# Optimization experiments

Measured on AMD Instinct MI355X. Metric: run time of the kernel, lower is better.

Reference implementation:

```python
import jax, jax.numpy as jnp
import numpy as np

N_NODES = 100000


def setup_inputs() -> dict:
    key = jax.random.key(0)
    k1, k2, k3, k4 = jax.random.split(key, 4)
    E = 1600000
    in_dim, out_dim = 256, 64
    h = jax.random.normal(k1, (N_NODES, in_dim), dtype=jnp.float32)
    src = jax.random.randint(k2, (E,), 0, N_NODES, dtype=jnp.int64)
    dst = jax.random.randint(k3, (E,), 0, N_NODES, dtype=jnp.int64)
    W = jax.random.normal(k4, (in_dim, out_dim), dtype=jnp.float32) * (1.0 / np.sqrt(in_dim))
    b = jnp.zeros((out_dim,), dtype=jnp.float32)
    return {"h": h, "src": src, "dst": dst, "W": W, "b": b}


def reference(h, src, dst, W, b):
    # dgl GraphConv, norm='both': out = D_in^{-1/2} A D_out^{-1/2} h W + b
    E = src.shape[0]
    ones = jnp.ones((E,), dtype=h.dtype)
    deg_out = jax.ops.segment_sum(ones, src, num_segments=N_NODES)  # out-degree of src nodes
    deg_in = jax.ops.segment_sum(ones, dst, num_segments=N_NODES)   # in-degree of dst nodes
    norm_src = jnp.clip(deg_out, 1.0, None) ** -0.5                  # [N]
    norm_dst = jnp.clip(deg_in, 1.0, None) ** -0.5                   # [N]
    # in_dim > out_dim: project first (as dgl does), then aggregate small features
    x = (h * norm_src[:, None]) @ W                                  # [N, out_dim]
    msgs = x[src]                                                    # [E, out_dim] gather
    agg = jax.ops.segment_sum(msgs, dst, num_segments=N_NODES)      # [N, out_dim] scatter-add
    out = agg * norm_dst[:, None] + b
    # ReLU; dropout is identity in eval mode
    return jax.nn.relu(out)
```

## Files before the change

### kernel.cpp

```cpp
#include <hip/hip_runtime.h>
#include <hip/hip_fp16.h>

#define N_NODES 100000
#define IN_DIM 256
#define OUT_DIM 64
#define NT 782
#define NB 256
#define SCHUNK 4096
#define SB ((NT * NB + SCHUNK - 1) / SCHUNK)
#define SCAN_M (NT * NB)

typedef _Float16 half8 __attribute__((ext_vector_type(8)));
typedef float f32x4 __attribute__((ext_vector_type(4)));

__global__ __launch_bounds__(256) void count_kernel(const int* __restrict__ src,
                                                    const int* __restrict__ dst,
                                                    int* __restrict__ CD, int* __restrict__ CS,
                                                    int E, int chunk) {
    __shared__ int hd[NT], hs[NT];
    const int t = threadIdx.x, blk = blockIdx.x;
    for (int i = t; i < NT; i += 256) { hd[i] = 0; hs[i] = 0; }
    __syncthreads();
    const int lo = blk * chunk;
    int hi = lo + chunk; if (hi > E) hi = E;
    for (int i = lo + t; i < hi; i += 256) {
        atomicAdd(&hd[dst[i] >> 7], 1);
        atomicAdd(&hs[src[i] >> 7], 1);
    }
    __syncthreads();
    for (int i = t; i < NT; i += 256) {
        CD[i * NB + blk] = hd[i];
        CS[i * NB + blk] = hs[i];
    }
}

__global__ __launch_bounds__(256) void scan_blocks_kernel(int* __restrict__ CD, int* __restrict__ CS,
                                                          int* __restrict__ BSD, int* __restrict__ BSS) {
    int cid = blockIdx.x;
    int* arr; int* bs;
    if (cid < SB) { arr = CD; bs = BSD; } else { arr = CS; bs = BSS; cid -= SB; }
    const int t = threadIdx.x;
    const int base = cid * SCHUNK + t * 16;
    int pre[16];
    int s = 0;
#pragma unroll
    for (int r = 0; r < 16; ++r) {
        int v = (base + r < SCAN_M) ? arr[base + r] : 0;
        pre[r] = s; s += v;
    }
    const int lane = t & 63;
    int incl = s;
#pragma unroll
    for (int off = 1; off < 64; off <<= 1) {
        int y = __shfl_up(incl, off);
        if (lane >= off) incl += y;
    }
    int wave_excl = incl - s;
    __shared__ int wtot[4];
    if (lane == 63) wtot[t >> 6] = incl;
    __syncthreads();
    int woff = 0;
    for (int w = 0; w < (t >> 6); ++w) woff += wtot[w];
    int bexcl = woff + wave_excl;
#pragma unroll
    for (int r = 0; r < 16; ++r)
        if (base + r < SCAN_M) arr[base + r] = bexcl + pre[r];
    if (t == 0) bs[cid] = wtot[0] + wtot[1] + wtot[2] + wtot[3];
}

__device__ __forceinline__ void scan_chunk_sums(const int* __restrict__ BSD,
                                                const int* __restrict__ BSS,
                                                int* sBSD, int* sBSS, int t) {
    if (t < 128) {
        const int lane = t & 63;
        const int* bs = (t < 64) ? BSD : BSS;
        int* sb = (t < 64) ? sBSD : sBSS;
        int v = (lane < SB) ? bs[lane] : 0;
        int incl = v;
#pragma unroll
        for (int off = 1; off < 64; off <<= 1) {
            int y = __shfl_up(incl, off);
            if (lane >= off) incl += y;
        }
        if (lane < SB) sb[lane] = incl - v;
    }
}

__global__ __launch_bounds__(256) void scatter_kernel(const int* __restrict__ src,
                                                      const int* __restrict__ dst,
                                                      const int* __restrict__ CD, const int* __restrict__ CS,
                                                      const int* __restrict__ BSD, const int* __restrict__ BSS,
                                                      int* __restrict__ binnedD,
                                                      unsigned char* __restrict__ srcb,
                                                      int E, int chunk) {
    __shared__ int curD[NT], curS[NT];
    __shared__ int sBSD[SB], sBSS[SB];
    const int t = threadIdx.x, blk = blockIdx.x;
    scan_chunk_sums(BSD, BSS, sBSD, sBSS, t);
    __syncthreads();
    for (int i = t; i < NT; i += 256) {
        int idx = i * NB + blk;
        curD[i] = CD[idx] + sBSD[idx >> 12];
        curS[i] = CS[idx] + sBSS[idx >> 12];
    }
    __syncthreads();
    const int lo = blk * chunk;
    int hi = lo + chunk; if (hi > E) hi = E;
    for (int i = lo + t; i < hi; i += 256) {
        int s = src[i], d = dst[i];
        int p = atomicAdd(&curD[d >> 7], 1);
        binnedD[p] = (s << 7) | (d & 127);
        int ps = atomicAdd(&curS[s >> 7], 1);
        srcb[ps] = (unsigned char)(s & 127);
    }
}

__global__ __launch_bounds__(256) void tile_kernel(const int* __restrict__ CD, const int* __restrict__ CS,
                                                   const int* __restrict__ BSD, const int* __restrict__ BSS,
                                                   const int* __restrict__ binnedD,
                                                   const unsigned char* __restrict__ srcb,
                                                   int* __restrict__ csr,
                                                   int* __restrict__ offs, int* __restrict__ cnt,
                                                   int* __restrict__ deg_out, int E) {
    __shared__ int h[128], cur[128];
    __shared__ int w0tot;
    __shared__ int sBSD[SB], sBSS[SB];
    const int bin = blockIdx.x, t = threadIdx.x, lane = t & 63;
    const int i0 = bin * NB;

    scan_chunk_sums(BSD, BSS, sBSD, sBSS, t);
    if (t < 128) h[t] = 0;
    __syncthreads();

    const int base = CD[i0] + sBSD[i0 >> 12];
    const int next = (bin + 1 < NT) ? (CD[i0 + NB] + sBSD[(i0 + NB) >> 12]) : E;
    const int m = next - base;
    for (int k = t; k < m; k += 256) atomicAdd(&h[binnedD[base + k] & 127], 1);
    __syncthreads();
    int v = (t < 128) ? h[t] : 0;
    int incl = v;
#pragma unroll
    for (int off = 1; off < 64; off <<= 1) {
        int y = __shfl_up(incl, off);
        if (lane >= off) incl += y;
    }
    if (t == 63) w0tot = incl;
    __syncthreads();
    int excl = incl - v + ((t >= 64 && t < 128) ? w0tot : 0);
    if (t < 128) {
        cur[t] = excl;
        int node = bin * 128 + t;
        if (node < N_NODES) { offs[node] = base + excl; cnt[node] = v; }
    }
    __syncthreads();
    for (int k = t; k < m; k += 256) {
        int rec = binnedD[base + k];
        int p = atomicAdd(&cur[rec & 127], 1);
        csr[base + p] = rec >> 7;
    }

    __syncthreads();
    if (t < 128) h[t] = 0;
    __syncthreads();
    const int sb = CS[i0] + sBSS[i0 >> 12];
    const int sn = (bin + 1 < NT) ? (CS[i0 + NB] + sBSS[(i0 + NB) >> 12]) : E;
    const int sm = sn - sb;
    for (int k = t; k < sm; k += 256) atomicAdd(&h[srcb[sb + k]], 1);
    __syncthreads();
    if (t < 128) {
        int node = bin * 128 + t;
        if (node < N_NODES) deg_out[node] = h[t];
    }
}

#define B_LD 264
__global__ __launch_bounds__(256) void gemm_kernel(const float* __restrict__ hmat,
                                                   const float* __restrict__ W,
                                                   const int* __restrict__ deg_out,
                                                   __half* __restrict__ xh) {
    __shared__ _Float16 sB[64 * B_LD];
    const int t = threadIdx.x;
    const int lane = t & 63;
    const int w = t >> 6;
    const int row0 = blockIdx.x * 64;

#pragma unroll
    for (int it = 0; it < 16; ++it) {
        int f = t + it * 256;
        int k = f >> 4;
        int n4 = (f & 15) * 4;
        float4 v = *(const float4*)(W + (size_t)k * OUT_DIM + n4);
        sB[(n4 + 0) * B_LD + k] = (_Float16)v.x;
        sB[(n4 + 1) * B_LD + k] = (_Float16)v.y;
        sB[(n4 + 2) * B_LD + k] = (_Float16)v.z;
        sB[(n4 + 3) * B_LD + k] = (_Float16)v.w;
    }
    __syncthreads();

    const int m16 = lane & 15;
    const int kq = lane >> 4;
    int grow = row0 + w * 16 + m16;
    const float* arow = hmat + (size_t)(grow < N_NODES ? grow : N_NODES - 1) * IN_DIM;

    f32x4 acc[4] = {{0.f,0.f,0.f,0.f},{0.f,0.f,0.f,0.f},{0.f,0.f,0.f,0.f},{0.f,0.f,0.f,0.f}};

#pragma unroll
    for (int kb = 0; kb < 8; ++kb) {
        const int koff = kb * 32 + kq * 8;
        float4 alo = *(const float4*)(arow + koff);
        float4 ahi = *(const float4*)(arow + koff + 4);
        _Float16 af[8];
        af[0] = (_Float16)alo.x; af[1] = (_Float16)alo.y;
        af[2] = (_Float16)alo.z; af[3] = (_Float16)alo.w;
        af[4] = (_Float16)ahi.x; af[5] = (_Float16)ahi.y;
        af[6] = (_Float16)ahi.z; af[7] = (_Float16)ahi.w;
        half8 a = *(half8*)af;
#pragma unroll
        for (int ni = 0; ni < 4; ++ni) {
            half8 b = *(const half8*)&sB[(ni * 16 + m16) * B_LD + koff];
            acc[ni] = __builtin_amdgcn_mfma_f32_16x16x32_f16(a, b, acc[ni], 0, 0, 0);
        }
    }

    const int rq = kq * 4;
    float nrm[4];
#pragma unroll
    for (int r = 0; r < 4; ++r) {
        int row = row0 + w * 16 + rq + r;
        int d = (row < N_NODES) ? deg_out[row] : 1;
        nrm[r] = rsqrtf((float)(d < 1 ? 1 : d));
    }
#pragma unroll
    for (int ni = 0; ni < 4; ++ni) {
        int col = ni * 16 + m16;
#pragma unroll
        for (int r = 0; r < 4; ++r) {
            int row = row0 + w * 16 + rq + r;
            if (row < N_NODES)
                xh[(size_t)row * OUT_DIM + col] = __float2half(acc[ni][r] * nrm[r]);
        }
    }
}

__global__ __launch_bounds__(256) void aggregate_kernel(const int* __restrict__ offs,
                                                        const int* __restrict__ cnt,
                                                        const int* __restrict__ csr,
                                                        const __half* __restrict__ xh,
                                                        const float* __restrict__ b,
                                                        float* __restrict__ out) {
    const int t = threadIdx.x;
    const int lane = t & 63;
    const int wid = t >> 6;
    const int node = blockIdx.x * 4 + wid;
    const int g = lane >> 3;
    const int c = lane & 7;

    const int start = offs[node];
    const int n = cnt[node];

    float acc[8] = {0.f, 0.f, 0.f, 0.f, 0.f, 0.f, 0.f, 0.f};
    for (int base = 0; base < n; base += 64) {
        int k = base + lane;
        int sidx = (k < n) ? csr[start + k] : 0;
        int m = n - base; if (m > 64) m = 64;
        for (int rb = 0; rb < m; rb += 32) {
            uint4 raw[4]; float wq[4];
#pragma unroll
            for (int q = 0; q < 4; ++q) {
                int e = rb + 8 * q + g;
                int s = __shfl(sidx, e);
                bool val = e < m;
                s = val ? s : 0;
                wq[q] = val ? 1.f : 0.f;
                raw[q] = *(const uint4*)(xh + (size_t)s * OUT_DIM + 8 * c);
            }
#pragma unroll
            for (int q = 0; q < 4; ++q) {
                const __half2* hp = (const __half2*)&raw[q];
#pragma unroll
                for (int p = 0; p < 4; ++p) {
                    float2 f = __half22float2(hp[p]);
                    acc[2 * p]     = fmaf(wq[q], f.x, acc[2 * p]);
                    acc[2 * p + 1] = fmaf(wq[q], f.y, acc[2 * p + 1]);
                }
            }
        }
    }

#pragma unroll
    for (int off = 8; off < 64; off <<= 1) {
#pragma unroll
        for (int p = 0; p < 8; ++p)
            acc[p] += __shfl_xor(acc[p], off);
    }

    if (g == 0) {
        float nrm = rsqrtf((float)(n < 1 ? 1 : n));
        float4 bv0 = *(const float4*)&b[c * 8];
        float4 bv1 = *(const float4*)&b[c * 8 + 4];
        float4 r0, r1;
        r0.x = fmaxf(fmaf(acc[0], nrm, bv0.x), 0.f);
        r0.y = fmaxf(fmaf(acc[1], nrm, bv0.y), 0.f);
        r0.z = fmaxf(fmaf(acc[2], nrm, bv0.z), 0.f);
        r0.w = fmaxf(fmaf(acc[3], nrm, bv0.w), 0.f);
        r1.x = fmaxf(fmaf(acc[4], nrm, bv1.x), 0.f);
        r1.y = fmaxf(fmaf(acc[5], nrm, bv1.y), 0.f);
        r1.z = fmaxf(fmaf(acc[6], nrm, bv1.z), 0.f);
        r1.w = fmaxf(fmaf(acc[7], nrm, bv1.w), 0.f);
        float4* orow = (float4*)(out + (size_t)node * OUT_DIM + c * 8);
        orow[0] = r0;
        orow[1] = r1;
    }
}

extern "C" void kernel_launch(void* const* d_in, const int* in_sizes, int n_in,
                              void* d_out, int out_size, void* d_ws, size_t ws_size,
                              hipStream_t stream) {
    const float* h   = (const float*)d_in[0];
    const int*   src = (const int*)d_in[1];
    const int*   dst = (const int*)d_in[2];
    const float* W   = (const float*)d_in[3];
    const float* b   = (const float*)d_in[4];
    float* out = (float*)d_out;
    const int E = in_sizes[1];
    const int chunk = (E + NB - 1) / NB;

    char* ws = (char*)d_ws;
    int*           CD      = (int*)(ws);
    int*           CS      = (int*)(ws + 800768);
    int*           BSD     = (int*)(ws + 1601536);
    int*           BSS     = (int*)(ws + 1601792);
    int*           binnedD = (int*)(ws + 1602048);
    unsigned char* srcb    = (unsigned char*)(ws + 8002048);
    int*           csr     = (int*)(ws + 9602048);
    int*           offs    = (int*)(ws + 16002048);
    int*           cntA    = (int*)(ws + 16402048);
    int*           deg_out = (int*)(ws + 16802048);
    __half*        xh      = (__half*)(ws + 17202048);

    count_kernel<<<NB, 256, 0, stream>>>(src, dst, CD, CS, E, chunk);
    scan_blocks_kernel<<<2 * SB, 256, 0, stream>>>(CD, CS, BSD, BSS);
    scatter_kernel<<<NB, 256, 0, stream>>>(src, dst, CD, CS, BSD, BSS, binnedD, srcb, E, chunk);
    tile_kernel<<<NT, 256, 0, stream>>>(CD, CS, BSD, BSS, binnedD, srcb, csr, offs, cntA, deg_out, E);
    gemm_kernel<<<(N_NODES + 63) / 64, 256, 0, stream>>>(h, W, deg_out, xh);
    aggregate_kernel<<<N_NODES / 4, 256, 0, stream>>>(offs, cntA, csr, xh, b, out);
}
```

Before: 299.7 us.

## Fuse CSR build and GEMM into one cooperative kernel; apply src norm during aggregation

Merges the count, scan, scatter, tile and GEMM kernels into a single cooperative kernel with grid-wide syncs. Some blocks run the degree histogram while the others run the GEMM at the same time. Moving the source normalization into the aggregation gather is what removes the GEMM's dependence on the out-degree. The change also vectorizes edge loads as int4 and uses smaller scan chunks. The cost is grid.sync overhead, an extra norm_src load per gathered edge, and a host-side occupancy query on every launch.

```diff
diff --git a/kernel.cpp b/kernel.cpp
--- a/kernel.cpp
+++ b/kernel.cpp
@@ -1,243 +1,268 @@
 #include <hip/hip_runtime.h>
 #include <hip/hip_fp16.h>
+#include <hip/hip_cooperative_groups.h>
+
+namespace cg = cooperative_groups;
 
 #define N_NODES 100000
 #define IN_DIM 256
 #define OUT_DIM 64
 #define NT 782
 #define NB 256
-#define SCHUNK 4096
-#define SB ((NT * NB + SCHUNK - 1) / SCHUNK)
 #define SCAN_M (NT * NB)
+#define NCH 196
+#define GRID 1024
+#define B_LD 264
 
 typedef _Float16 half8 __attribute__((ext_vector_type(8)));
 typedef float f32x4 __attribute__((ext_vector_type(4)));
 
-__global__ __launch_bounds__(256) void count_kernel(const int* __restrict__ src,
-                                                    const int* __restrict__ dst,
-                                                    int* __restrict__ CD, int* __restrict__ CS,
-                                                    int E, int chunk) {
-    __shared__ int hd[NT], hs[NT];
-    const int t = threadIdx.x, blk = blockIdx.x;
-    for (int i = t; i < NT; i += 256) { hd[i] = 0; hs[i] = 0; }
-    __syncthreads();
-    const int lo = blk * chunk;
-    int hi = lo + chunk; if (hi > E) hi = E;
-    for (int i = lo + t; i < hi; i += 256) {
-        atomicAdd(&hd[dst[i] >> 7], 1);
-        atomicAdd(&hs[src[i] >> 7], 1);
-    }
-    __syncthreads();
-    for (int i = t; i < NT; i += 256) {
-        CD[i * NB + blk] = hd[i];
-        CS[i * NB + blk] = hs[i];
-    }
-}
-
-__global__ __launch_bounds__(256) void scan_blocks_kernel(int* __restrict__ CD, int* __restrict__ CS,
-                                                          int* __restrict__ BSD, int* __restrict__ BSS) {
-    int cid = blockIdx.x;
-    int* arr; int* bs;
-    if (cid < SB) { arr = CD; bs = BSD; } else { arr = CS; bs = BSS; cid -= SB; }
-    const int t = threadIdx.x;
-    const int base = cid * SCHUNK + t * 16;
-    int pre[16];
-    int s = 0;
-#pragma unroll
-    for (int r = 0; r < 16; ++r) {
-        int v = (base + r < SCAN_M) ? arr[base + r] : 0;
-        pre[r] = s; s += v;
-    }
-    const int lane = t & 63;
-    int incl = s;
+__device__ __forceinline__ void bscan_nch(const int* __restrict__ g, int* __restrict__ out,
+                                          int* wt, int t) {
+    const int lane = t & 63, wv = t >> 6;
+    int v = (t < NCH) ? g[t] : 0;
+    int incl = v;
 #pragma unroll
     for (int off = 1; off < 64; off <<= 1) {
         int y = __shfl_up(incl, off);
         if (lane >= off) incl += y;
     }
-    int wave_excl = incl - s;
-    __shared__ int wtot[4];
-    if (lane == 63) wtot[t >> 6] = incl;
+    if (lane == 63) wt[wv] = incl;
     __syncthreads();
     int woff = 0;
-    for (int w = 0; w < (t >> 6); ++w) woff += wtot[w];
-    int bexcl = woff + wave_excl;
-#pragma unroll
-    for (int r = 0; r < 16; ++r)
-        if (base + r < SCAN_M) arr[base + r] = bexcl + pre[r];
-    if (t == 0) bs[cid] = wtot[0] + wtot[1] + wtot[2] + wtot[3];
+    for (int x = 0; x < wv; ++x) woff += wt[x];
+    if (t < NCH) out[t] = woff + incl - v;
+    __syncthreads();
 }
 
-__device__ __forceinline__ void scan_chunk_sums(const int* __restrict__ BSD,
-                                                const int* __restrict__ BSS,
-                                                int* sBSD, int* sBSS, int t) {
-    if (t < 128) {
-        const int lane = t & 63;
-        const int* bs = (t < 64) ? BSD : BSS;
-        int* sb = (t < 64) ? sBSD : sBSS;
-        int v = (lane < SB) ? bs[lane] : 0;
-        int incl = v;
-#pragma unroll
-        for (int off = 1; off < 64; off <<= 1) {
-            int y = __shfl_up(incl, off);
-            if (lane >= off) incl += y;
-        }
-        if (lane < SB) sb[lane] = incl - v;
-    }
-}
-
-__global__ __launch_bounds__(256) void scatter_kernel(const int* __restrict__ src,
-                                                      const int* __restrict__ dst,
-                                                      const int* __restrict__ CD, const int* __restrict__ CS,
-                                                      const int* __restrict__ BSD, const int* __restrict__ BSS,
-                                                      int* __restrict__ binnedD,
-                                                      unsigned char* __restrict__ srcb,
-                                                      int E, int chunk) {
-    __shared__ int curD[NT], curS[NT];
-    __shared__ int sBSD[SB], sBSS[SB];
-    const int t = threadIdx.x, blk = blockIdx.x;
-    scan_chunk_sums(BSD, BSS, sBSD, sBSS, t);
-    __syncthreads();
-    for (int i = t; i < NT; i += 256) {
-        int idx = i * NB + blk;
-        curD[i] = CD[idx] + sBSD[idx >> 12];
-        curS[i] = CS[idx] + sBSS[idx >> 12];
-    }
-    __syncthreads();
-    const int lo = blk * chunk;
-    int hi = lo + chunk; if (hi > E) hi = E;
-    for (int i = lo + t; i < hi; i += 256) {
-        int s = src[i], d = dst[i];
-        int p = atomicAdd(&curD[d >> 7], 1);
-        binnedD[p] = (s << 7) | (d & 127);
-        int ps = atomicAdd(&curS[s >> 7], 1);
-        srcb[ps] = (unsigned char)(s & 127);
-    }
-}
-
-__global__ __launch_bounds__(256) void tile_kernel(const int* __restrict__ CD, const int* __restrict__ CS,
-                                                   const int* __restrict__ BSD, const int* __restrict__ BSS,
-                                                   const int* __restrict__ binnedD,
-                                                   const unsigned char* __restrict__ srcb,
-                                                   int* __restrict__ csr,
-                                                   int* __restrict__ offs, int* __restrict__ cnt,
-                                                   int* __restrict__ deg_out, int E) {
-    __shared__ int h[128], cur[128];
-    __shared__ int w0tot;
-    __shared__ int sBSD[SB], sBSS[SB];
-    const int bin = blockIdx.x, t = threadIdx.x, lane = t & 63;
-    const int i0 = bin * NB;
-
-    scan_chunk_sums(BSD, BSS, sBSD, sBSS, t);
-    if (t < 128) h[t] = 0;
-    __syncthreads();
-
-    const int base = CD[i0] + sBSD[i0 >> 12];
-    const int next = (bin + 1 < NT) ? (CD[i0 + NB] + sBSD[(i0 + NB) >> 12]) : E;
-    const int m = next - base;
-    for (int k = t; k < m; k += 256) atomicAdd(&h[binnedD[base + k] & 127], 1);
-    __syncthreads();
-    int v = (t < 128) ? h[t] : 0;
-    int incl = v;
-#pragma unroll
-    for (int off = 1; off < 64; off <<= 1) {
-        int y = __shfl_up(incl, off);
-        if (lane >= off) incl += y;
-    }
-    if (t == 63) w0tot = incl;
-    __syncthreads();
-    int excl = incl - v + ((t >= 64 && t < 128) ? w0tot : 0);
-    if (t < 128) {
-        cur[t] = excl;
-        int node = bin * 128 + t;
-        if (node < N_NODES) { offs[node] = base + excl; cnt[node] = v; }
-    }
-    __syncthreads();
-    for (int k = t; k < m; k += 256) {
-        int rec = binnedD[base + k];
-        int p = atomicAdd(&cur[rec & 127], 1);
-        csr[base + p] = rec >> 7;
-    }
-
-    __syncthreads();
-    if (t < 128) h[t] = 0;
-    __syncthreads();
-    const int sb = CS[i0] + sBSS[i0 >> 12];
-    const int sn = (bin + 1 < NT) ? (CS[i0 + NB] + sBSS[(i0 + NB) >> 12]) : E;
-    const int sm = sn - sb;
-    for (int k = t; k < sm; k += 256) atomicAdd(&h[srcb[sb + k]], 1);
-    __syncthreads();
-    if (t < 128) {
-        int node = bin * 128 + t;
-        if (node < N_NODES) deg_out[node] = h[t];
-    }
-}
-
-#define B_LD 264
-__global__ __launch_bounds__(256) void gemm_kernel(const float* __restrict__ hmat,
-                                                   const float* __restrict__ W,
-                                                   const int* __restrict__ deg_out,
-                                                   __half* __restrict__ xh) {
-    __shared__ _Float16 sB[64 * B_LD];
+__global__ __launch_bounds__(256, 4) void coop_kernel(
+        const int* __restrict__ src, const int* __restrict__ dst,
+        const float* __restrict__ hmat, const float* __restrict__ W,
+        int* __restrict__ CD, int* __restrict__ CS,
+        int* __restrict__ BSD, int* __restrict__ BSS,
+        int* __restrict__ binnedD, unsigned char* __restrict__ srcb,
+        int* __restrict__ csr, int* __restrict__ offs, int* __restrict__ cnt,
+        float* __restrict__ norm_src, __half* __restrict__ xh,
+        int E, int CH4) {
+    cg::grid_group grid = cg::this_grid();
+    __shared__ __align__(16) char smem[64 * B_LD * 2];
     const int t = threadIdx.x;
+    const int blk = blockIdx.x;
     const int lane = t & 63;
-    const int w = t >> 6;
-    const int row0 = blockIdx.x * 64;
-
-#pragma unroll
-    for (int it = 0; it < 16; ++it) {
-        int f = t + it * 256;
-        int k = f >> 4;
-        int n4 = (f & 15) * 4;
-        float4 v = *(const float4*)(W + (size_t)k * OUT_DIM + n4);
-        sB[(n4 + 0) * B_LD + k] = (_Float16)v.x;
-        sB[(n4 + 1) * B_LD + k] = (_Float16)v.y;
-        sB[(n4 + 2) * B_LD + k] = (_Float16)v.z;
-        sB[(n4 + 3) * B_LD + k] = (_Float16)v.w;
-    }
-    __syncthreads();
-
-    const int m16 = lane & 15;
-    const int kq = lane >> 4;
-    int grow = row0 + w * 16 + m16;
-    const float* arow = hmat + (size_t)(grow < N_NODES ? grow : N_NODES - 1) * IN_DIM;
-
-    f32x4 acc[4] = {{0.f,0.f,0.f,0.f},{0.f,0.f,0.f,0.f},{0.f,0.f,0.f,0.f},{0.f,0.f,0.f,0.f}};
-
-#pragma unroll
-    for (int kb = 0; kb < 8; ++kb) {
-        const int koff = kb * 32 + kq * 8;
-        float4 alo = *(const float4*)(arow + koff);
-        float4 ahi = *(const float4*)(arow + koff + 4);
-        _Float16 af[8];
-        af[0] = (_Float16)alo.x; af[1] = (_Float16)alo.y;
-        af[2] = (_Float16)alo.z; af[3] = (_Float16)alo.w;
-        af[4] = (_Float16)ahi.x; af[5] = (_Float16)ahi.y;
-        af[6] = (_Float16)ahi.z; af[7] = (_Float16)ahi.w;
-        half8 a = *(half8*)af;
-#pragma unroll
-        for (int ni = 0; ni < 4; ++ni) {
-            half8 b = *(const half8*)&sB[(ni * 16 + m16) * B_LD + koff];
-            acc[ni] = __builtin_amdgcn_mfma_f32_16x16x32_f16(a, b, acc[ni], 0, 0, 0);
-        }
-    }
-
-    const int rq = kq * 4;
-    float nrm[4];
-#pragma unroll
-    for (int r = 0; r < 4; ++r) {
-        int row = row0 + w * 16 + rq + r;
-        int d = (row < N_NODES) ? deg_out[row] : 1;
-        nrm[r] = rsqrtf((float)(d < 1 ? 1 : d));
-    }
-#pragma unroll
-    for (int ni = 0; ni < 4; ++ni) {
-        int col = ni * 16 + m16;
-#pragma unroll
-        for (int r = 0; r < 4; ++r) {
-            int row = row0 + w * 16 + rq + r;
-            if (row < N_NODES)
-                xh[(size_t)row * OUT_DIM + col] = __float2half(acc[ni][r] * nrm[r]);
+    const int wv = t >> 6;
+    const int nblk = gridDim.x;
+
+    if (blk < NB) {
+        int* hd = (int*)smem;
+        int* hs = hd + NT;
+        for (int i = t; i < NT; i += 256) { hd[i] = 0; hs[i] = 0; }
+        __syncthreads();
+        const int E4 = E >> 2;
+        const int lo4 = blk * CH4;
+        int hi4 = lo4 + CH4; if (hi4 > E4) hi4 = E4;
+        const int4* s4 = (const int4*)src;
+        const int4* d4 = (const int4*)dst;
+        for (int k = lo4 + t; k < hi4; k += 256) {
+            int4 a = s4[k], c = d4[k];
+            atomicAdd(&hs[a.x >> 7], 1); atomicAdd(&hs[a.y >> 7], 1);
+            atomicAdd(&hs[a.z >> 7], 1); atomicAdd(&hs[a.w >> 7], 1);
+            atomicAdd(&hd[c.x >> 7], 1); atomicAdd(&hd[c.y >> 7], 1);
+            atomicAdd(&hd[c.z >> 7], 1); atomicAdd(&hd[c.w >> 7], 1);
+        }
+        if (blk == NB - 1) {
+            for (int i = E4 * 4 + t; i < E; i += 256) {
+                atomicAdd(&hs[src[i] >> 7], 1);
+                atomicAdd(&hd[dst[i] >> 7], 1);
+            }
+        }
+        __syncthreads();
+        for (int i = t; i < NT; i += 256) {
+            CD[i * NB + blk] = hd[i];
+            CS[i * NB + blk] = hs[i];
+        }
+    } else {
+        _Float16* sB = (_Float16*)smem;
+#pragma unroll
+        for (int it = 0; it < 16; ++it) {
+            int f = t + it * 256;
+            int k = f >> 4;
+            int n4 = (f & 15) * 4;
+            float4 v = *(const float4*)(W + (size_t)k * OUT_DIM + n4);
+            sB[(n4 + 0) * B_LD + k] = (_Float16)v.x;
+            sB[(n4 + 1) * B_LD + k] = (_Float16)v.y;
+            sB[(n4 + 2) * B_LD + k] = (_Float16)v.z;
+            sB[(n4 + 3) * B_LD + k] = (_Float16)v.w;
+        }
+        __syncthreads();
+        const int m16 = lane & 15;
+        const int kq = lane >> 4;
+        const int gw = (blk - NB) * 4 + wv;
+        const int gstride = (nblk - NB) * 4;
+        for (int u = gw; u < N_NODES / 16; u += gstride) {
+            const float* arow = hmat + (size_t)(u * 16 + m16) * IN_DIM;
+            f32x4 acc[4] = {{0,0,0,0},{0,0,0,0},{0,0,0,0},{0,0,0,0}};
+#pragma unroll
+            for (int kb = 0; kb < 8; ++kb) {
+                const int koff = kb * 32 + kq * 8;
+                float4 alo = *(const float4*)(arow + koff);
+                float4 ahi = *(const float4*)(arow + koff + 4);
+                _Float16 af[8];
+                af[0] = (_Float16)alo.x; af[1] = (_Float16)alo.y;
+                af[2] = (_Float16)alo.z; af[3] = (_Float16)alo.w;
+                af[4] = (_Float16)ahi.x; af[5] = (_Float16)ahi.y;
+                af[6] = (_Float16)ahi.z; af[7] = (_Float16)ahi.w;
+                half8 a = *(half8*)af;
+#pragma unroll
+                for (int ni = 0; ni < 4; ++ni) {
+                    half8 b = *(const half8*)&sB[(ni * 16 + m16) * B_LD + koff];
+                    acc[ni] = __builtin_amdgcn_mfma_f32_16x16x32_f16(a, b, acc[ni], 0, 0, 0);
+                }
+            }
+            const int rq = kq * 4;
+#pragma unroll
+            for (int ni = 0; ni < 4; ++ni) {
+                int col = ni * 16 + m16;
+#pragma unroll
+                for (int r = 0; r < 4; ++r) {
+                    int row = u * 16 + rq + r;
+                    xh[(size_t)row * OUT_DIM + col] = __float2half(acc[ni][r]);
+                }
+            }
+        }
+    }
+    grid.sync();
+
+    {
+        int* wt = (int*)smem;
+        for (int c = blk; c < 2 * NCH; c += nblk) {
+            int* arr = (c < NCH) ? CD : CS;
+            int* bs  = (c < NCH) ? BSD : BSS;
+            int cid  = (c < NCH) ? c : c - NCH;
+            int base = cid * 1024 + t * 4;
+            int pre[4], s = 0;
+#pragma unroll
+            for (int r = 0; r < 4; ++r) {
+                int v = (base + r < SCAN_M) ? arr[base + r] : 0;
+                pre[r] = s; s += v;
+            }
+            int incl = s;
+#pragma unroll
+            for (int off = 1; off < 64; off <<= 1) {
+                int y = __shfl_up(incl, off);
+                if (lane >= off) incl += y;
+            }
+            if (lane == 63) wt[wv] = incl;
+            __syncthreads();
+            int woff = 0;
+            for (int x = 0; x < wv; ++x) woff += wt[x];
+            int bexcl = woff + incl - s;
+#pragma unroll
+            for (int r = 0; r < 4; ++r)
+                if (base + r < SCAN_M) arr[base + r] = bexcl + pre[r];
+            if (t == 0) bs[cid] = wt[0] + wt[1] + wt[2] + wt[3];
+            __syncthreads();
+        }
+    }
+    grid.sync();
+
+    if (blk < NB) {
+        int* curD = (int*)smem;
+        int* curS = curD + NT;
+        int* sBSD = curS + NT;
+        int* sBSS = sBSD + 256;
+        int* wt   = sBSS + 256;
+        bscan_nch(BSD, sBSD, wt, t);
+        bscan_nch(BSS, sBSS, wt, t);
+        for (int i = t; i < NT; i += 256) {
+            int idx = i * NB + blk;
+            curD[i] = CD[idx] + sBSD[idx >> 10];
+            curS[i] = CS[idx] + sBSS[idx >> 10];
+        }
+        __syncthreads();
+        const int E4 = E >> 2;
+        const int lo4 = blk * CH4;
+        int hi4 = lo4 + CH4; if (hi4 > E4) hi4 = E4;
+        const int4* s4 = (const int4*)src;
+        const int4* d4 = (const int4*)dst;
+        for (int k = lo4 + t; k < hi4; k += 256) {
+            int4 a = s4[k], c = d4[k];
+            int p;
+            p = atomicAdd(&curD[c.x >> 7], 1); binnedD[p] = (a.x << 7) | (c.x & 127);
+            p = atomicAdd(&curD[c.y >> 7], 1); binnedD[p] = (a.y << 7) | (c.y & 127);
+            p = atomicAdd(&curD[c.z >> 7], 1); binnedD[p] = (a.z << 7) | (c.z & 127);
+            p = atomicAdd(&curD[c.w >> 7], 1); binnedD[p] = (a.w << 7) | (c.w & 127);
+            p = atomicAdd(&curS[a.x >> 7], 1); srcb[p] = (unsigned char)(a.x & 127);
+            p = atomicAdd(&curS[a.y >> 7], 1); srcb[p] = (unsigned char)(a.y & 127);
+            p = atomicAdd(&curS[a.z >> 7], 1); srcb[p] = (unsigned char)(a.z & 127);
+            p = atomicAdd(&curS[a.w >> 7], 1); srcb[p] = (unsigned char)(a.w & 127);
+        }
+        if (blk == NB - 1) {
+            for (int i = E4 * 4 + t; i < E; i += 256) {
+                int s = src[i], d = dst[i];
+                int p = atomicAdd(&curD[d >> 7], 1);
+                binnedD[p] = (s << 7) | (d & 127);
+                int ps = atomicAdd(&curS[s >> 7], 1);
+                srcb[ps] = (unsigned char)(s & 127);
+            }
+        }
+    }
+    grid.sync();
+
+    {
+        int* hh   = (int*)smem;
+        int* cur  = hh + 128;
+        int* sBSD = cur + 128;
+        int* sBSS = sBSD + 224;
+        int* wt   = sBSS + 224;
+        int* w0t  = wt + 4;
+        bscan_nch(BSD, sBSD, wt, t);
+        bscan_nch(BSS, sBSS, wt, t);
+        for (int bin = blk; bin < NT; bin += nblk) {
+            const int i0 = bin * NB;
+            if (t < 128) hh[t] = 0;
+            __syncthreads();
+            const int base = CD[i0] + sBSD[i0 >> 10];
+            const int next = (bin + 1 < NT) ? (CD[i0 + NB] + sBSD[(i0 + NB) >> 10]) : E;
+            const int m = next - base;
+            for (int k = t; k < m; k += 256) atomicAdd(&hh[binnedD[base + k] & 127], 1);
+            __syncthreads();
+            int v = (t < 128) ? hh[t] : 0;
+            int incl = v;
+#pragma unroll
+            for (int off = 1; off < 64; off <<= 1) {
+                int y = __shfl_up(incl, off);
+                if (lane >= off) incl += y;
+            }
+            if (t == 63) *w0t = incl;
+            __syncthreads();
+            int excl = incl - v + ((t >= 64 && t < 128) ? *w0t : 0);
+            if (t < 128) {
+                cur[t] = excl;
+                int node = bin * 128 + t;
+                if (node < N_NODES) { offs[node] = base + excl; cnt[node] = v; }
+            }
+            __syncthreads();
+            for (int k = t; k < m; k += 256) {
+                int rec = binnedD[base + k];
+                int p = atomicAdd(&cur[rec & 127], 1);
+                csr[base + p] = rec >> 7;
+            }
+            __syncthreads();
+            if (t < 128) hh[t] = 0;
+            __syncthreads();
+            const int sb = CS[i0] + sBSS[i0 >> 10];
+            const int sn = (bin + 1 < NT) ? (CS[i0 + NB] + sBSS[(i0 + NB) >> 10]) : E;
+            const int sm = sn - sb;
+            for (int k = t; k < sm; k += 256) atomicAdd(&hh[srcb[sb + k]], 1);
+            __syncthreads();
+            if (t < 128) {
+                int node = bin * 128 + t;
+                if (node < N_NODES) {
+                    int d = hh[t];
+                    norm_src[node] = rsqrtf((float)(d < 1 ? 1 : d));
+                }
+            }
+            __syncthreads();
         }
     }
 }
@@ -246,6 +271,7 @@
                                                         const int* __restrict__ cnt,
                                                         const int* __restrict__ csr,
                                                         const __half* __restrict__ xh,
+                                                        const float* __restrict__ norm_src,
                                                         const float* __restrict__ b,
                                                         float* __restrict__ out) {
     const int t = threadIdx.x;
@@ -271,7 +297,8 @@
                 int s = __shfl(sidx, e);
                 bool val = e < m;
                 s = val ? s : 0;
-                wq[q] = val ? 1.f : 0.f;
+                float ns = norm_src[s];
+                wq[q] = val ? ns : 0.f;
                 raw[q] = *(const uint4*)(xh + (size_t)s * OUT_DIM + 8 * c);
             }
 #pragma unroll
@@ -322,26 +349,36 @@
     const float* W   = (const float*)d_in[3];
     const float* b   = (const float*)d_in[4];
     float* out = (float*)d_out;
-    const int E = in_sizes[1];
-    const int chunk = (E + NB - 1) / NB;
+    int E = in_sizes[1];
+    int CH4 = ((E >> 2) + NB - 1) / NB;
 
     char* ws = (char*)d_ws;
-    int*           CD      = (int*)(ws);
-    int*           CS      = (int*)(ws + 800768);
-    int*           BSD     = (int*)(ws + 1601536);
-    int*           BSS     = (int*)(ws + 1601792);
-    int*           binnedD = (int*)(ws + 1602048);
-    unsigned char* srcb    = (unsigned char*)(ws + 8002048);
-    int*           csr     = (int*)(ws + 9602048);
-    int*           offs    = (int*)(ws + 16002048);
-    int*           cntA    = (int*)(ws + 16402048);
-    int*           deg_out = (int*)(ws + 16802048);
-    __half*        xh      = (__half*)(ws + 17202048);
-
-    count_kernel<<<NB, 256, 0, stream>>>(src, dst, CD, CS, E, chunk);
-    scan_blocks_kernel<<<2 * SB, 256, 0, stream>>>(CD, CS, BSD, BSS);
-    scatter_kernel<<<NB, 256, 0, stream>>>(src, dst, CD, CS, BSD, BSS, binnedD, srcb, E, chunk);
-    tile_kernel<<<NT, 256, 0, stream>>>(CD, CS, BSD, BSS, binnedD, srcb, csr, offs, cntA, deg_out, E);
-    gemm_kernel<<<(N_NODES + 63) / 64, 256, 0, stream>>>(h, W, deg_out, xh);
-    aggregate_kernel<<<N_NODES / 4, 256, 0, stream>>>(offs, cntA, csr, xh, b, out);
+    int*           CD       = (int*)(ws);
+    int*           CS       = (int*)(ws + 800768);
+    int*           BSD      = (int*)(ws + 1601536);
+    int*           BSS      = (int*)(ws + 1602560);
+    int*           binnedD  = (int*)(ws + 1603584);
+    unsigned char* srcb     = (unsigned char*)(ws + 8003584);
+    int*           csr      = (int*)(ws + 9603584);
+    int*           offs     = (int*)(ws + 16003584);
+    int*           cntA     = (int*)(ws + 16403584);
+    float*         norm_src = (float*)(ws + 16803584);
+    __half*        xh       = (__half*)(ws + 17203584);
+
+    int maxB = 4;
+    hipOccupancyMaxActiveBlocksPerMultiprocessor(&maxB, (const void*)coop_kernel, 256, 0);
+    if (maxB < 1) maxB = 1;
+    int gridBlocks = 256 * maxB;
+    if (gridBlocks > GRID) gridBlocks = GRID;
+    if (gridBlocks <= NB) gridBlocks = NB + 256;
+
+    void* cargs[] = {(void*)&src, (void*)&dst, (void*)&h, (void*)&W,
+                     (void*)&CD, (void*)&CS, (void*)&BSD, (void*)&BSS,
+                     (void*)&binnedD, (void*)&srcb, (void*)&csr,
+                     (void*)&offs, (void*)&cntA, (void*)&norm_src, (void*)&xh,
+                     (void*)&E, (void*)&CH4};
+    hipLaunchCooperativeKernel((const void*)coop_kernel, dim3(gridBlocks), dim3(256),
+                               cargs, 0, stream);
+
+    aggregate_kernel<<<N_NODES / 4, 256, 0, stream>>>(offs, cntA, csr, xh, norm_src, b, out);
 }
```

New measurement: 506.8 us. 69.1% more time.
